# Optimization experiments

Measured on AMD Instinct MI355X. Metric: run time of the kernel, lower is better.

The kernel has to match this reference:

```python
import jax, jax.numpy as jnp
import numpy as np

N_E = 4096
E_DIM = 256
DECAY = 0.99
EPS = 1e-5


def setup_inputs() -> dict:
    key = jax.random.key(0)
    k1, k2 = jax.random.split(key)
    z = jax.random.normal(k1, (8, 256, 16, 16, 16), dtype=jnp.float32)
    embedding = jax.random.normal(k2, (N_E, E_DIM), dtype=jnp.float32)
    return {
        "z": z,
        "embedding": embedding,
        "cluster_size": jnp.zeros((N_E,), dtype=jnp.float32),
        "embedding_avg": embedding,  # buffer initialized as embedding.clone()
    }


def reference(z, embedding, cluster_size, embedding_avg):
    n_e, e_dim = embedding.shape
    # b c h w d -> b h w d c, then flatten tokens
    zt = jnp.einsum('bchwd->bhwdc', z)
    zf = zt.reshape(-1, e_dim)                      # [N, e_dim]
    # squared euclidean distances: ||z||^2 + ||e||^2 - 2 z.e
    d = (jnp.sum(zf * zf, axis=1, keepdims=True)
         + jnp.sum(embedding * embedding, axis=1)
         - 2.0 * jnp.einsum('bd,nd->bn', zf, embedding))  # [N, n_e]
    idx = jnp.argmin(d, axis=1)                     # [N]
    # EMA statistics (equivalent to one-hot.T reductions, done via scatter)
    n_total = jnp.zeros((n_e,), zf.dtype).at[idx].add(1.0)          # encodings.sum(0)
    dw = jax.ops.segment_sum(zf, idx, num_segments=n_e)             # encodings.T @ zf
    new_cluster = cluster_size * DECAY + (1.0 - DECAY) * n_total
    new_avg = embedding_avg * DECAY + (1.0 - DECAY) * dw
    n = new_cluster.sum()
    cs = (new_cluster + EPS) / (n + n_e * EPS) * n
    new_embed = new_avg / cs[:, None]
    # quantize (gather == one-hot @ embedding) with straight-through estimator
    zq = jnp.take(embedding, idx, axis=0).reshape(zt.shape)
    zq = zt + jax.lax.stop_gradient(zq - zt)
    zq = jnp.einsum('bhwdc->bchwd', zq)
    usage = (n_total > 0).sum().astype(jnp.float32) / n_e
    return zq, idx, new_cluster, new_avg, new_embed, usage
```

## Files before the change

### kernel.cpp

```cpp
#include <hip/hip_runtime.h>

#define N_E   4096
#define E_DIM 256
#define NTOK  32768
#define ZX    4096
#define DECAY 0.99f
#define EPSV  1e-5f
#define TAU   0.3f
#define NJB   32
#define NHALF 64
#define NSPL  4
#define IBIG  0x7fffffff

typedef _Float16 half8 __attribute__((ext_vector_type(8)));
typedef __attribute__((ext_vector_type(4))) float f32x4;

__device__ __forceinline__ unsigned short f2h(float x) {
    _Float16 h = (_Float16)x;
    unsigned short u;
    __builtin_memcpy(&u, &h, 2);
    return u;
}
__device__ __forceinline__ float h2f(unsigned short u) {
    _Float16 h;
    __builtin_memcpy(&h, &u, 2);
    return (float)h;
}
__device__ __forceinline__ unsigned umin2(unsigned a, unsigned b) { return a < b ? a : b; }
__device__ __forceinline__ unsigned umax2(unsigned a, unsigned b) { return a > b ? a : b; }
__device__ __forceinline__ void gload16(const void* g, void* l) {
    __builtin_amdgcn_global_load_lds(
        (const __attribute__((address_space(1))) char*)g,
        (__attribute__((address_space(3))) char*)l, 16, 0, 0);
}

__global__ void k_prep_z(const float* __restrict__ z, unsigned short* __restrict__ zh) {
    __shared__ float lt[64][65];
    const int bid = blockIdx.x;
    const int xt = bid & 63, ct = (bid >> 6) & 3, b = bid >> 8;
    const int tid = threadIdx.x;
    #pragma unroll
    for (int r = 0; r < 4; ++r) {
        int cy = r * 16 + (tid >> 4);
        int xx4 = tid & 15;
        float4 v = ((const float4*)z)[(size_t)(b * 256 + ct * 64 + cy) * 1024 + xt * 16 + xx4];
        lt[cy][xx4 * 4 + 0] = v.x; lt[cy][xx4 * 4 + 1] = v.y;
        lt[cy][xx4 * 4 + 2] = v.z; lt[cy][xx4 * 4 + 3] = v.w;
    }
    __syncthreads();
    #pragma unroll
    for (int it = 0; it < 2; ++it) {
        int tl = it * 32 + (tid >> 3);
        int c8 = tid & 7;
        unsigned short h[8];
        #pragma unroll
        for (int u = 0; u < 8; ++u) h[u] = f2h(lt[c8 * 8 + u][tl]);
        size_t t = (size_t)(b * 4096 + xt * 64 + tl);
        size_t o = t * 256 + ct * 64 + c8 * 8;
        *(ushort4*)&zh[o]     = make_ushort4(h[0], h[1], h[2], h[3]);
        *(ushort4*)&zh[o + 4] = make_ushort4(h[4], h[5], h[6], h[7]);
    }
}

__global__ void k_prep_e(const float* __restrict__ emb, unsigned short* __restrict__ Bp,
                         float* __restrict__ enorm32, double* __restrict__ enorm64,
                         int* __restrict__ cnt, int* __restrict__ flagCnt,
                         int* __restrict__ flagCnt2) {
    if (threadIdx.x < 4) cnt[blockIdx.x * 4 + threadIdx.x] = 0;
    if (blockIdx.x == 0 && threadIdx.x == 0) { *flagCnt = 0; *flagCnt2 = 0; }
    int j = blockIdx.x * 4 + (threadIdx.x >> 6);
    int lane = threadIdx.x & 63;
    float4 v = ((const float4*)emb)[(size_t)j * 64 + lane];
    float f[4] = {v.x, v.y, v.z, v.w};
    unsigned short h[4];
    #pragma unroll
    for (int u = 0; u < 4; ++u) h[u] = f2h(f[u]);
    *(ushort4*)&Bp[(size_t)j * E_DIM + lane * 4] = make_ushort4(h[0], h[1], h[2], h[3]);
    double s = 0.0;
    #pragma unroll
    for (int u = 0; u < 4; ++u) s += (double)f[u] * (double)f[u];
    #pragma unroll
    for (int off = 32; off; off >>= 1) s += __shfl_down(s, off, 64);
    if (lane == 0) { enorm32[j] = (float)s; enorm64[j] = s; }
}

__global__ __launch_bounds__(256) void k_dist(
        const unsigned short* __restrict__ zh,
        const unsigned short* __restrict__ Bp, const float* __restrict__ enorm32,
        unsigned* __restrict__ pk1, unsigned* __restrict__ pk2, unsigned* __restrict__ pk3) {
    __shared__ __align__(16) char smem[32768];
    const int tid = threadIdx.x;
    const int lane = tid & 63;
    const int w = tid >> 6;
    const int wr = w >> 1, wc = w & 1;
    const int t0 = blockIdx.x * 128;
    const int jb = blockIdx.y;
    const int j0 = jb * 128;
    const int sw16 = (((lane & 7) ^ (lane >> 3)) << 4);
    const int rowsub = lane >> 3;

    f32x4 acc[4][4];
    #pragma unroll
    for (int m = 0; m < 4; ++m)
        #pragma unroll
        for (int nn = 0; nn < 4; ++nn)
            acc[m][nn] = (f32x4){0.f, 0.f, 0.f, 0.f};

    auto stage = [&](int s) {
        const int kb = s * 128 + sw16;
        #pragma unroll
        for (int c = 0; c < 4; ++c) {
            int seg = w * 4 + c;
            int arow = t0 + seg * 8 + rowsub;
            int brow = j0 + seg * 8 + rowsub;
            gload16((const char*)zh + (size_t)arow * 512 + kb, &smem[seg * 1024]);
            gload16((const char*)Bp + (size_t)brow * 512 + kb, &smem[16384 + seg * 1024]);
        }
    };

    stage(0);
    for (int s = 0; s < 4; ++s) {
        __syncthreads();
        const int xr = ((lane & 7) << 4);
        #pragma unroll
        for (int kk = 0; kk < 2; ++kk) {
            const int colb = (kk * 64 + ((lane >> 4) << 4)) ^ xr;
            half8 a[4], b[4];
            #pragma unroll
            for (int m = 0; m < 4; ++m)
                a[m] = *(const half8*)&smem[((wr * 64 + m * 16 + (lane & 15)) << 7) + colb];
            #pragma unroll
            for (int nn = 0; nn < 4; ++nn)
                b[nn] = *(const half8*)&smem[16384 + ((wc * 64 + nn * 16 + (lane & 15)) << 7) + colb];
            #pragma unroll
            for (int m = 0; m < 4; ++m)
                #pragma unroll
                for (int nn = 0; nn < 4; ++nn)
                    acc[m][nn] = __builtin_amdgcn_mfma_f32_16x16x32_f16(b[nn], a[m], acc[m][nn], 0, 0, 0);
        }
        if (s < 3) {
            __syncthreads();
            stage(s + 1);
        }
    }

    const int g   = lane >> 4;
    const int gg4 = g * 4;
    const int h   = jb * 2 + wc;
    float enb[4][4];
    #pragma unroll
    for (int nn = 0; nn < 4; ++nn) {
        float4 e4 = *(const float4*)&enorm32[j0 + wc * 64 + nn * 16 + gg4];
        enb[nn][0] = e4.x + 4096.f; enb[nn][1] = e4.y + 4096.f;
        enb[nn][2] = e4.z + 4096.f; enb[nn][3] = e4.w + 4096.f;
    }
    unsigned s1 = 0, s2 = 0, s3 = 0;
    #pragma unroll
    for (int m = 0; m < 4; ++m) {
        unsigned k1 = 0xFFFFFFFFu, k2 = 0xFFFFFFFFu, k3 = 0xFFFFFFFFu;
        #pragma unroll
        for (int nn = 0; nn < 4; ++nn)
            #pragma unroll
            for (int r = 0; r < 4; ++r) {
                float sc = fmaf(-2.f, acc[m][nn][r], enb[nn][r]);
                unsigned key = (__float_as_uint(sc) & 0xFFFFFFC0u)
                             | (unsigned)(gg4 + nn * 16 + r);
                k3 = umin2(k3, umax2(k2, key));
                k2 = umin2(k2, umax2(k1, key));
                k1 = umin2(k1, key);
            }
        #pragma unroll
        for (int off = 16; off <= 32; off <<= 1) {
            unsigned b1 = (unsigned)__shfl_xor((int)k1, off, 64);
            unsigned b2 = (unsigned)__shfl_xor((int)k2, off, 64);
            unsigned b3 = (unsigned)__shfl_xor((int)k3, off, 64);
            unsigned p  = umax2(k1, b1);
            unsigned q  = umin2(k2, b2);
            unsigned r2 = umax2(k2, b2);
            unsigned ss = umin2(k3, b3);
            k1 = umin2(k1, b1);
            k2 = umin2(p, q);
            k3 = umin2(umax2(p, q), umin2(r2, ss));
        }
        s1 = (g == m) ? k1 : s1;
        s2 = (g == m) ? k2 : s2;
        s3 = (g == m) ? k3 : s3;
    }
    size_t o = (size_t)h * NTOK + t0 + wr * 64 + lane;
    pk1[o] = s1; pk2[o] = s2; pk3[o] = s3;
}

__global__ void k_merge(const unsigned* __restrict__ pk1, const unsigned* __restrict__ pk2,
                        const unsigned* __restrict__ pk3,
                        int* __restrict__ idx32, int* __restrict__ cnt,
                        float* __restrict__ out_idx,
                        int* __restrict__ xlist, int* __restrict__ xn,
                        int* __restrict__ flagList, int* __restrict__ flagCount,
                        int* __restrict__ flagList2, int* __restrict__ flagCount2) {
    int t = blockIdx.x * blockDim.x + threadIdx.x;
    if (t >= NTOK) return;
    unsigned g1 = 0xFFFFFFFFu, g2 = 0xFFFFFFFFu;
    int h1 = 0;
    for (int s = 0; s < NHALF; s++) {
        unsigned a = pk1[(size_t)s * NTOK + t];
        unsigned b = pk2[(size_t)s * NTOK + t];
        bool c = a < g1;
        g2 = c ? g1 : umin2(g2, a);
        h1 = c ? s : h1;
        g1 = c ? a : g1;
        g2 = umin2(g2, b);
    }
    int x1 = h1 * 64 + (int)(g1 & 63u);
    idx32[t] = x1;
    atomicAdd(&cnt[x1], 1);
    out_idx[t] = (float)x1;
    float v1 = __uint_as_float(g1 & 0xFFFFFFC0u);
    float v2 = __uint_as_float(g2 & 0xFFFFFFC0u);
    if (v2 - v1 >= TAU) return;
    unsigned thrk = __float_as_uint(v1 + TAU) | 63u;
    int nc = 0; bool full = false;
    for (int s = 0; s < NHALF; s++) {
        unsigned a = pk1[(size_t)s * NTOK + t];
        if (a > thrk) continue;
        if (pk3[(size_t)s * NTOK + t] <= thrk) { full = true; break; }
        if (nc == 8) { full = true; break; }
        xlist[t * 8 + nc++] = s * 64 + (int)(a & 63u);
        unsigned b = pk2[(size_t)s * NTOK + t];
        if (b <= thrk) {
            if (nc == 8) { full = true; break; }
            xlist[t * 8 + nc++] = s * 64 + (int)(b & 63u);
        }
    }
    if (full) {
        int q = atomicAdd(flagCount2, 1);
        flagList2[q] = t;
    } else {
        xn[t] = nc;
        int q = atomicAdd(flagCount, 1);
        flagList[q] = t;
    }
}

__global__ void k_tri(const float* __restrict__ z, const float* __restrict__ emb,
                      const double* __restrict__ enorm64,
                      const int* __restrict__ flagList, const int* __restrict__ flagCount,
                      const int* __restrict__ xlist, const int* __restrict__ xn,
                      int* __restrict__ idx32, int* __restrict__ cnt,
                      float* __restrict__ out_idx) {
    const int lane = threadIdx.x & 63;
    const int wid = blockIdx.x * (blockDim.x >> 6) + (threadIdx.x >> 6);
    const int nw = gridDim.x * (blockDim.x >> 6);
    const int nf = *flagCount;
    for (int f = wid; f < nf; f += nw) {
        int t = flagList[f];
        int b = t >> 12, x = t & 4095;
        double zz[4];
        #pragma unroll
        for (int u = 0; u < 4; ++u)
            zz[u] = (double)z[(size_t)(b * 256 + lane * 4 + u) * 4096 + x];
        int m = xn[t];
        double best = 1e300; int bi = IBIG;
        for (int c = 0; c < m; ++c) {
            int j = xlist[t * 8 + c];
            float4 e = ((const float4*)emb)[(size_t)j * 64 + lane];
            double d = zz[0] * (double)e.x + zz[1] * (double)e.y
                     + zz[2] * (double)e.z + zz[3] * (double)e.w;
            #pragma unroll
            for (int off = 32; off; off >>= 1) d += __shfl_down(d, off, 64);
            double s = enorm64[j] - 2.0 * d;
            if (s < best || (s == best && j < bi)) { best = s; bi = j; }
        }
        if (lane == 0) {
            int old = idx32[t];
            if (bi != old) {
                idx32[t] = bi;
                out_idx[t] = (float)bi;
                atomicSub(&cnt[old], 1);
                atomicAdd(&cnt[bi], 1);
            }
        }
    }
}

__global__ void k_recheck(const float* __restrict__ z, const float* __restrict__ emb,
                          const double* __restrict__ enorm64,
                          const int* __restrict__ flagList, const int* __restrict__ flagCount,
                          int* __restrict__ idx32, int* __restrict__ cnt,
                          float* __restrict__ out_idx) {
    __shared__ float zrow[E_DIM];
    __shared__ double rv[1024];
    __shared__ int ri[1024];
    const int tid = threadIdx.x;
    const int nf = *flagCount;
    for (int f = blockIdx.x; f < nf; f += gridDim.x) {
        const int t = flagList[f];
        const int b = t >> 12, x = t & 4095;
        __syncthreads();
        if (tid < E_DIM) zrow[tid] = z[(size_t)(b * 256 + tid) * 4096 + x];
        __syncthreads();
        double best = 1e300; int bi = IBIG;
        for (int s = 0; s < N_E / 1024; s++) {
            int j = s * 1024 + tid;
            const float4* er4 = (const float4*)(emb + (size_t)j * E_DIM);
            double a0 = 0.0, a1 = 0.0, a2 = 0.0, a3 = 0.0;
            for (int k4 = 0; k4 < 64; ++k4) {
                float4 e = er4[k4];
                a0 = fma((double)e.x, (double)zrow[k4 * 4 + 0], a0);
                a1 = fma((double)e.y, (double)zrow[k4 * 4 + 1], a1);
                a2 = fma((double)e.z, (double)zrow[k4 * 4 + 2], a2);
                a3 = fma((double)e.w, (double)zrow[k4 * 4 + 3], a3);
            }
            double d = enorm64[j] - 2.0 * ((a0 + a1) + (a2 + a3));
            if (d < best || (d == best && j < bi)) { best = d; bi = j; }
        }
        rv[tid] = best; ri[tid] = bi;
        __syncthreads();
        for (int off = 512; off; off >>= 1) {
            if (tid < off) {
                if (rv[tid + off] < rv[tid] ||
                    (rv[tid + off] == rv[tid] && ri[tid + off] < ri[tid])) {
                    rv[tid] = rv[tid + off]; ri[tid] = ri[tid + off];
                }
            }
            __syncthreads();
        }
        if (tid == 0) {
            int old = idx32[t];
            int nw = ri[0];
            if (nw != old) {
                idx32[t] = nw;
                out_idx[t] = (float)nw;
                atomicSub(&cnt[old], 1);
                atomicAdd(&cnt[nw], 1);
            }
        }
        __syncthreads();
    }
}

__global__ void k_scan(const int* __restrict__ cnt, int* __restrict__ offs,
                       const float* __restrict__ cluster_size,
                       float* __restrict__ nval, float* __restrict__ out_usage) {
    __shared__ int sc[1024];
    __shared__ float sn[1024];
    __shared__ float su[1024];
    int tid = threadIdx.x;
    int c0 = cnt[tid * 4], c1 = cnt[tid * 4 + 1], c2 = cnt[tid * 4 + 2], c3 = cnt[tid * 4 + 3];
    int ls = c0 + c1 + c2 + c3;
    float ns = 0.f, us = 0.f;
    {
        int cc[4] = {c0, c1, c2, c3};
        #pragma unroll
        for (int u = 0; u < 4; ++u) {
            ns += cluster_size[tid * 4 + u] * DECAY + (1.f - DECAY) * (float)cc[u];
            us += (cc[u] > 0) ? 1.f : 0.f;
        }
    }
    sc[tid] = ls; sn[tid] = ns; su[tid] = us;
    __syncthreads();
    for (int off = 1; off < 1024; off <<= 1) {
        int v = (tid >= off) ? sc[tid - off] : 0;
        __syncthreads();
        sc[tid] += v;
        __syncthreads();
    }
    int base = sc[tid] - ls;
    offs[tid * 4] = base;
    offs[tid * 4 + 1] = base + c0;
    offs[tid * 4 + 2] = base + c0 + c1;
    offs[tid * 4 + 3] = base + c0 + c1 + c2;
    for (int off = 512; off; off >>= 1) {
        if (tid < off) { sn[tid] += sn[tid + off]; su[tid] += su[tid + off]; }
        __syncthreads();
    }
    if (tid == 0) { *nval = sn[0]; *out_usage = su[0] / (float)N_E; }
}

__global__ void k_place(const int* __restrict__ idx32, int* __restrict__ offs,
                        int* __restrict__ tokList) {
    int t = blockIdx.x * blockDim.x + threadIdx.x;
    if (t >= NTOK) return;
    int j = idx32[t];
    int p = atomicAdd(&offs[j], 1);
    tokList[p] = t;
}

__global__ __launch_bounds__(512) void k_dw(const unsigned short* __restrict__ zh,
                       const int* __restrict__ cnt, const int* __restrict__ offs,
                       const int* __restrict__ tokList, float* __restrict__ dwp) {
    __shared__ float red[8][256];
    const int j = blockIdx.x;
    const int split = blockIdx.y;
    const int g = threadIdx.x >> 6;
    const int lane = threadIdx.x & 63;
    const int n = cnt[j];
    const int s0 = offs[j] - n;
    const int stride = NSPL * 8;
    float4 acc = make_float4(0.f, 0.f, 0.f, 0.f);
    int i = split * 8 + g;
    if (i < n) {
        int t_cur = tokList[s0 + i];
        i += stride;
        for (; i < n; i += stride) {
            int t_nxt = tokList[s0 + i];
            ushort4 h = *(const ushort4*)&zh[(size_t)t_cur * 256 + lane * 4];
            acc.x += h2f(h.x); acc.y += h2f(h.y);
            acc.z += h2f(h.z); acc.w += h2f(h.w);
            t_cur = t_nxt;
        }
        ushort4 h = *(const ushort4*)&zh[(size_t)t_cur * 256 + lane * 4];
        acc.x += h2f(h.x); acc.y += h2f(h.y);
        acc.z += h2f(h.z); acc.w += h2f(h.w);
    }
    red[g][lane * 4 + 0] = acc.x; red[g][lane * 4 + 1] = acc.y;
    red[g][lane * 4 + 2] = acc.z; red[g][lane * 4 + 3] = acc.w;
    __syncthreads();
    if (g == 0) {
        float4 o;
        int c = lane * 4;
        o.x = red[0][c+0] + red[1][c+0] + red[2][c+0] + red[3][c+0]
            + red[4][c+0] + red[5][c+0] + red[6][c+0] + red[7][c+0];
        o.y = red[0][c+1] + red[1][c+1] + red[2][c+1] + red[3][c+1]
            + red[4][c+1] + red[5][c+1] + red[6][c+1] + red[7][c+1];
        o.z = red[0][c+2] + red[1][c+2] + red[2][c+2] + red[3][c+2]
            + red[4][c+2] + red[5][c+2] + red[6][c+2] + red[7][c+2];
        o.w = red[0][c+3] + red[1][c+3] + red[2][c+3] + red[3][c+3]
            + red[4][c+3] + red[5][c+3] + red[6][c+3] + red[7][c+3];
        ((float4*)dwp)[((size_t)split * N_E + j) * 64 + lane] = o;
    }
}

__global__ void k_final(const float* __restrict__ dwp, const int* __restrict__ cnt,
                        const float* __restrict__ cluster_size,
                        const float* __restrict__ emb_avg, const float* __restrict__ nval,
                        float* __restrict__ out_cluster, float* __restrict__ out_avg,
                        float* __restrict__ out_embed) {
    int j = blockIdx.x * 4 + (threadIdx.x >> 6);
    int lane = threadIdx.x & 63;
    float4 dw = make_float4(0.f, 0.f, 0.f, 0.f);
    #pragma unroll
    for (int s = 0; s < NSPL; ++s) {
        float4 v = ((const float4*)dwp)[((size_t)s * N_E + j) * 64 + lane];
        dw.x += v.x; dw.y += v.y; dw.z += v.z; dw.w += v.w;
    }
    float nc = cluster_size[j] * DECAY + (1.f - DECAY) * (float)cnt[j];
    float nv = *nval;
    float cs = (nc + EPSV) / (nv + (float)N_E * EPSV) * nv;
    float4 ea = ((const float4*)emb_avg)[(size_t)j * 64 + lane];
    float4 na, ne;
    na.x = ea.x * DECAY + (1.f - DECAY) * dw.x;
    na.y = ea.y * DECAY + (1.f - DECAY) * dw.y;
    na.z = ea.z * DECAY + (1.f - DECAY) * dw.z;
    na.w = ea.w * DECAY + (1.f - DECAY) * dw.w;
    ne.x = na.x / cs; ne.y = na.y / cs; ne.z = na.z / cs; ne.w = na.w / cs;
    ((float4*)out_avg)[(size_t)j * 64 + lane] = na;
    ((float4*)out_embed)[(size_t)j * 64 + lane] = ne;
    if (lane == 0) out_cluster[j] = nc;
}

__global__ void k_zq(const float* __restrict__ emb, const int* __restrict__ idx32,
                     float* __restrict__ out_zq) {
    int t0 = blockIdx.x * 16;
    int b = t0 >> 12, x0 = t0 & 4095;
    int c4 = threadIdx.x >> 2;
    int xq = threadIdx.x & 3;
    int jj[4];
    #pragma unroll
    for (int i = 0; i < 4; ++i) jj[i] = idx32[t0 + xq * 4 + i];
    float4 e[4];
    #pragma unroll
    for (int i = 0; i < 4; ++i)
        e[i] = ((const float4*)emb)[(size_t)jj[i] * 64 + c4];
    float* ob = out_zq + (size_t)b * (E_DIM * ZX) + x0 + xq * 4;
    {
        float4 v = make_float4(e[0].x, e[1].x, e[2].x, e[3].x);
        *(float4*)&ob[(size_t)(c4 * 4 + 0) * ZX] = v;
    }
    {
        float4 v = make_float4(e[0].y, e[1].y, e[2].y, e[3].y);
        *(float4*)&ob[(size_t)(c4 * 4 + 1) * ZX] = v;
    }
    {
        float4 v = make_float4(e[0].z, e[1].z, e[2].z, e[3].z);
        *(float4*)&ob[(size_t)(c4 * 4 + 2) * ZX] = v;
    }
    {
        float4 v = make_float4(e[0].w, e[1].w, e[2].w, e[3].w);
        *(float4*)&ob[(size_t)(c4 * 4 + 3) * ZX] = v;
    }
}

extern "C" void kernel_launch(void* const* d_in, const int* in_sizes, int n_in,
                              void* d_out, int out_size, void* d_ws, size_t ws_size,
                              hipStream_t stream) {
    const float* z            = (const float*)d_in[0];
    const float* emb          = (const float*)d_in[1];
    const float* cluster_size = (const float*)d_in[2];
    const float* emb_avg      = (const float*)d_in[3];
    float* out = (float*)d_out;

    char* ws = (char*)d_ws;
    unsigned short* zh   = (unsigned short*)(ws + 0);
    float* enorm32       = (float*)(ws + 16777216);
    double* enorm64      = (double*)(ws + 16793600);
    int* idx32           = (int*)(ws + 16826368);
    int* flagList        = (int*)(ws + 16957440);
    int* flagList2       = (int*)(ws + 17088512);
    int* xlist           = (int*)(ws + 17219584);
    int* xn              = (int*)(ws + 18268160);
    int* cnt             = (int*)(ws + 18399232);
    int* offs            = (int*)(ws + 18415616);
    int* flagCnt         = (int*)(ws + 18432000);
    int* flagCnt2        = (int*)(ws + 18432064);
    float* nval          = (float*)(ws + 18432128);

    unsigned* pk1        = (unsigned*)(out + 0);
    unsigned* pk2        = (unsigned*)(out + 2097152);
    unsigned* pk3        = (unsigned*)(out + 4194304);
    float* dwp           = out + 0;
    unsigned short* Bp   = (unsigned short*)(out + 7340032);
    int*   tokList       = (int*)(out + 7864320);

    float* out_zq      = out + 0;
    float* out_idx     = out + 8388608;
    float* out_cluster = out + 8421376;
    float* out_avg     = out + 8425472;
    float* out_embed   = out + 9474048;
    float* out_usage   = out + 10522624;

    hipLaunchKernelGGL(k_prep_z, dim3(2048), dim3(256), 0, stream, z, zh);
    hipLaunchKernelGGL(k_prep_e, dim3(1024), dim3(256), 0, stream, emb, Bp, enorm32, enorm64,
                       cnt, flagCnt, flagCnt2);
    hipLaunchKernelGGL(k_dist,   dim3(256, NJB), dim3(256), 0, stream,
                       zh, Bp, enorm32, pk1, pk2, pk3);
    hipLaunchKernelGGL(k_merge,  dim3(128), dim3(256), 0, stream,
                       pk1, pk2, pk3, idx32, cnt, out_idx,
                       xlist, xn, flagList, flagCnt, flagList2, flagCnt2);
    hipLaunchKernelGGL(k_tri,    dim3(512), dim3(256), 0, stream,
                       z, emb, enorm64, flagList, flagCnt, xlist, xn, idx32, cnt, out_idx);
    hipLaunchKernelGGL(k_recheck, dim3(128), dim3(1024), 0, stream,
                       z, emb, enorm64, flagList2, flagCnt2, idx32, cnt, out_idx);
    hipLaunchKernelGGL(k_scan,   dim3(1), dim3(1024), 0, stream, cnt, offs,
                       cluster_size, nval, out_usage);
    hipLaunchKernelGGL(k_place,  dim3(128), dim3(256), 0, stream, idx32, offs, tokList);
    hipLaunchKernelGGL(k_dw,     dim3(4096, NSPL), dim3(512), 0, stream,
                       zh, cnt, offs, tokList, dwp);
    hipLaunchKernelGGL(k_final,  dim3(1024), dim3(256), 0, stream,
                       dwp, cnt, cluster_size, emb_avg, nval,
                       out_cluster, out_avg, out_embed);
    hipLaunchKernelGGL(k_zq,     dim3(2048), dim3(256), 0, stream, emb, idx32, out_zq);
}
```

Measured before the change: 201.7 us.

## Merge prep, refinement, and final/zq kernels to cut launch count

Result: no change. 199.8 us (-1.0%).

```diff
diff --git a/kernel.cpp b/kernel.cpp
--- a/kernel.cpp
+++ b/kernel.cpp
@@ -34,54 +34,56 @@
         (__attribute__((address_space(3))) char*)l, 16, 0, 0);
 }
 
-__global__ void k_prep_z(const float* __restrict__ z, unsigned short* __restrict__ zh) {
+__global__ void k_prep(const float* __restrict__ z, unsigned short* __restrict__ zh,
+                       const float* __restrict__ emb, unsigned short* __restrict__ Bp,
+                       float* __restrict__ enorm32, double* __restrict__ enorm64,
+                       int* __restrict__ cnt, int* __restrict__ flagCnt,
+                       int* __restrict__ flagCnt2) {
     __shared__ float lt[64][65];
-    const int bid = blockIdx.x;
-    const int xt = bid & 63, ct = (bid >> 6) & 3, b = bid >> 8;
     const int tid = threadIdx.x;
-    #pragma unroll
-    for (int r = 0; r < 4; ++r) {
-        int cy = r * 16 + (tid >> 4);
-        int xx4 = tid & 15;
-        float4 v = ((const float4*)z)[(size_t)(b * 256 + ct * 64 + cy) * 1024 + xt * 16 + xx4];
-        lt[cy][xx4 * 4 + 0] = v.x; lt[cy][xx4 * 4 + 1] = v.y;
-        lt[cy][xx4 * 4 + 2] = v.z; lt[cy][xx4 * 4 + 3] = v.w;
-    }
-    __syncthreads();
-    #pragma unroll
-    for (int it = 0; it < 2; ++it) {
-        int tl = it * 32 + (tid >> 3);
-        int c8 = tid & 7;
-        unsigned short h[8];
-        #pragma unroll
-        for (int u = 0; u < 8; ++u) h[u] = f2h(lt[c8 * 8 + u][tl]);
-        size_t t = (size_t)(b * 4096 + xt * 64 + tl);
-        size_t o = t * 256 + ct * 64 + c8 * 8;
-        *(ushort4*)&zh[o]     = make_ushort4(h[0], h[1], h[2], h[3]);
-        *(ushort4*)&zh[o + 4] = make_ushort4(h[4], h[5], h[6], h[7]);
-    }
-}
-
-__global__ void k_prep_e(const float* __restrict__ emb, unsigned short* __restrict__ Bp,
-                         float* __restrict__ enorm32, double* __restrict__ enorm64,
-                         int* __restrict__ cnt, int* __restrict__ flagCnt,
-                         int* __restrict__ flagCnt2) {
-    if (threadIdx.x < 4) cnt[blockIdx.x * 4 + threadIdx.x] = 0;
-    if (blockIdx.x == 0 && threadIdx.x == 0) { *flagCnt = 0; *flagCnt2 = 0; }
-    int j = blockIdx.x * 4 + (threadIdx.x >> 6);
-    int lane = threadIdx.x & 63;
-    float4 v = ((const float4*)emb)[(size_t)j * 64 + lane];
-    float f[4] = {v.x, v.y, v.z, v.w};
-    unsigned short h[4];
-    #pragma unroll
-    for (int u = 0; u < 4; ++u) h[u] = f2h(f[u]);
-    *(ushort4*)&Bp[(size_t)j * E_DIM + lane * 4] = make_ushort4(h[0], h[1], h[2], h[3]);
-    double s = 0.0;
-    #pragma unroll
-    for (int u = 0; u < 4; ++u) s += (double)f[u] * (double)f[u];
-    #pragma unroll
-    for (int off = 32; off; off >>= 1) s += __shfl_down(s, off, 64);
-    if (lane == 0) { enorm32[j] = (float)s; enorm64[j] = s; }
+    if (blockIdx.x < 2048) {
+        const int bid = blockIdx.x;
+        const int xt = bid & 63, ct = (bid >> 6) & 3, b = bid >> 8;
+        #pragma unroll
+        for (int r = 0; r < 4; ++r) {
+            int cy = r * 16 + (tid >> 4);
+            int xx4 = tid & 15;
+            float4 v = ((const float4*)z)[(size_t)(b * 256 + ct * 64 + cy) * 1024 + xt * 16 + xx4];
+            lt[cy][xx4 * 4 + 0] = v.x; lt[cy][xx4 * 4 + 1] = v.y;
+            lt[cy][xx4 * 4 + 2] = v.z; lt[cy][xx4 * 4 + 3] = v.w;
+        }
+        __syncthreads();
+        #pragma unroll
+        for (int it = 0; it < 2; ++it) {
+            int tl = it * 32 + (tid >> 3);
+            int c8 = tid & 7;
+            unsigned short h[8];
+            #pragma unroll
+            for (int u = 0; u < 8; ++u) h[u] = f2h(lt[c8 * 8 + u][tl]);
+            size_t t = (size_t)(b * 4096 + xt * 64 + tl);
+            size_t o = t * 256 + ct * 64 + c8 * 8;
+            *(ushort4*)&zh[o]     = make_ushort4(h[0], h[1], h[2], h[3]);
+            *(ushort4*)&zh[o + 4] = make_ushort4(h[4], h[5], h[6], h[7]);
+        }
+    } else {
+        const int eb = blockIdx.x - 2048;
+        if (tid < 4) cnt[eb * 4 + tid] = 0;
+        if (eb == 0 && tid == 0) { *flagCnt = 0; *flagCnt2 = 0; }
+        int j = eb * 4 + (tid >> 6);
+        int lane = tid & 63;
+        float4 v = ((const float4*)emb)[(size_t)j * 64 + lane];
+        float f[4] = {v.x, v.y, v.z, v.w};
+        unsigned short h[4];
+        #pragma unroll
+        for (int u = 0; u < 4; ++u) h[u] = f2h(f[u]);
+        *(ushort4*)&Bp[(size_t)j * E_DIM + lane * 4] = make_ushort4(h[0], h[1], h[2], h[3]);
+        double s = 0.0;
+        #pragma unroll
+        for (int u = 0; u < 4; ++u) s += (double)f[u] * (double)f[u];
+        #pragma unroll
+        for (int off = 32; off; off >>= 1) s += __shfl_down(s, off, 64);
+        if (lane == 0) { enorm32[j] = (float)s; enorm64[j] = s; }
+    }
 }
 
 __global__ __launch_bounds__(256) void k_dist(
@@ -201,6 +203,7 @@
     if (t >= NTOK) return;
     unsigned g1 = 0xFFFFFFFFu, g2 = 0xFFFFFFFFu;
     int h1 = 0;
+    #pragma unroll 4
     for (int s = 0; s < NHALF; s++) {
         unsigned a = pk1[(size_t)s * NTOK + t];
         unsigned b = pk2[(size_t)s * NTOK + t];
@@ -241,100 +244,97 @@
     }
 }
 
-__global__ void k_tri(const float* __restrict__ z, const float* __restrict__ emb,
-                      const double* __restrict__ enorm64,
-                      const int* __restrict__ flagList, const int* __restrict__ flagCount,
-                      const int* __restrict__ xlist, const int* __restrict__ xn,
-                      int* __restrict__ idx32, int* __restrict__ cnt,
-                      float* __restrict__ out_idx) {
-    const int lane = threadIdx.x & 63;
-    const int wid = blockIdx.x * (blockDim.x >> 6) + (threadIdx.x >> 6);
-    const int nw = gridDim.x * (blockDim.x >> 6);
-    const int nf = *flagCount;
-    for (int f = wid; f < nf; f += nw) {
-        int t = flagList[f];
-        int b = t >> 12, x = t & 4095;
-        double zz[4];
-        #pragma unroll
-        for (int u = 0; u < 4; ++u)
-            zz[u] = (double)z[(size_t)(b * 256 + lane * 4 + u) * 4096 + x];
-        int m = xn[t];
-        double best = 1e300; int bi = IBIG;
-        for (int c = 0; c < m; ++c) {
-            int j = xlist[t * 8 + c];
-            float4 e = ((const float4*)emb)[(size_t)j * 64 + lane];
-            double d = zz[0] * (double)e.x + zz[1] * (double)e.y
-                     + zz[2] * (double)e.z + zz[3] * (double)e.w;
+__global__ __launch_bounds__(512) void k_triR(
+        const float* __restrict__ z, const float* __restrict__ emb,
+        const double* __restrict__ enorm64,
+        const int* __restrict__ flagList, const int* __restrict__ flagCount,
+        const int* __restrict__ xlist, const int* __restrict__ xn,
+        const int* __restrict__ flagList2, const int* __restrict__ flagCount2,
+        int* __restrict__ idx32, int* __restrict__ cnt, float* __restrict__ out_idx) {
+    __shared__ float zrow[E_DIM];
+    __shared__ double rv[512];
+    __shared__ int ri[512];
+    const int tid = threadIdx.x;
+    if (blockIdx.x < 384) {
+        const int lane = tid & 63;
+        const int wid = blockIdx.x * 8 + (tid >> 6);
+        const int nw = 384 * 8;
+        const int nf = *flagCount;
+        for (int f = wid; f < nf; f += nw) {
+            int t = flagList[f];
+            int b = t >> 12, x = t & 4095;
+            double zz[4];
             #pragma unroll
-            for (int off = 32; off; off >>= 1) d += __shfl_down(d, off, 64);
-            double s = enorm64[j] - 2.0 * d;
-            if (s < best || (s == best && j < bi)) { best = s; bi = j; }
-        }
-        if (lane == 0) {
-            int old = idx32[t];
-            if (bi != old) {
-                idx32[t] = bi;
-                out_idx[t] = (float)bi;
-                atomicSub(&cnt[old], 1);
-                atomicAdd(&cnt[bi], 1);
+            for (int u = 0; u < 4; ++u)
+                zz[u] = (double)z[(size_t)(b * 256 + lane * 4 + u) * 4096 + x];
+            int m = xn[t];
+            double best = 1e300; int bi = IBIG;
+            for (int c = 0; c < m; ++c) {
+                int j = xlist[t * 8 + c];
+                float4 e = ((const float4*)emb)[(size_t)j * 64 + lane];
+                double d = zz[0] * (double)e.x + zz[1] * (double)e.y
+                         + zz[2] * (double)e.z + zz[3] * (double)e.w;
+                #pragma unroll
+                for (int off = 32; off; off >>= 1) d += __shfl_down(d, off, 64);
+                double s = enorm64[j] - 2.0 * d;
+                if (s < best || (s == best && j < bi)) { best = s; bi = j; }
             }
-        }
-    }
-}
-
-__global__ void k_recheck(const float* __restrict__ z, const float* __restrict__ emb,
-                          const double* __restrict__ enorm64,
-                          const int* __restrict__ flagList, const int* __restrict__ flagCount,
-                          int* __restrict__ idx32, int* __restrict__ cnt,
-                          float* __restrict__ out_idx) {
-    __shared__ float zrow[E_DIM];
-    __shared__ double rv[1024];
-    __shared__ int ri[1024];
-    const int tid = threadIdx.x;
-    const int nf = *flagCount;
-    for (int f = blockIdx.x; f < nf; f += gridDim.x) {
-        const int t = flagList[f];
-        const int b = t >> 12, x = t & 4095;
-        __syncthreads();
-        if (tid < E_DIM) zrow[tid] = z[(size_t)(b * 256 + tid) * 4096 + x];
-        __syncthreads();
-        double best = 1e300; int bi = IBIG;
-        for (int s = 0; s < N_E / 1024; s++) {
-            int j = s * 1024 + tid;
-            const float4* er4 = (const float4*)(emb + (size_t)j * E_DIM);
-            double a0 = 0.0, a1 = 0.0, a2 = 0.0, a3 = 0.0;
-            for (int k4 = 0; k4 < 64; ++k4) {
-                float4 e = er4[k4];
-                a0 = fma((double)e.x, (double)zrow[k4 * 4 + 0], a0);
-                a1 = fma((double)e.y, (double)zrow[k4 * 4 + 1], a1);
-                a2 = fma((double)e.z, (double)zrow[k4 * 4 + 2], a2);
-                a3 = fma((double)e.w, (double)zrow[k4 * 4 + 3], a3);
+            if (lane == 0) {
+                int old = idx32[t];
+                if (bi != old) {
+                    idx32[t] = bi;
+                    out_idx[t] = (float)bi;
+                    atomicSub(&cnt[old], 1);
+                    atomicAdd(&cnt[bi], 1);
+                }
             }
-            double d = enorm64[j] - 2.0 * ((a0 + a1) + (a2 + a3));
-            if (d < best || (d == best && j < bi)) { best = d; bi = j; }
-        }
-        rv[tid] = best; ri[tid] = bi;
-        __syncthreads();
-        for (int off = 512; off; off >>= 1) {
-            if (tid < off) {
-                if (rv[tid + off] < rv[tid] ||
-                    (rv[tid + off] == rv[tid] && ri[tid + off] < ri[tid])) {
-                    rv[tid] = rv[tid + off]; ri[tid] = ri[tid + off];
+        }
+    } else {
+        const int nf = *flagCount2;
+        for (int f = blockIdx.x - 384; f < nf; f += 128) {
+            const int t = flagList2[f];
+            const int b = t >> 12, x = t & 4095;
+            __syncthreads();
+            if (tid < E_DIM) zrow[tid] = z[(size_t)(b * 256 + tid) * 4096 + x];
+            __syncthreads();
+            double best = 1e300; int bi = IBIG;
+            for (int s = 0; s < N_E / 512; s++) {
+                int j = s * 512 + tid;
+                const float4* er4 = (const float4*)(emb + (size_t)j * E_DIM);
+                double a0 = 0.0, a1 = 0.0, a2 = 0.0, a3 = 0.0;
+                for (int k4 = 0; k4 < 64; ++k4) {
+                    float4 e = er4[k4];
+                    a0 = fma((double)e.x, (double)zrow[k4 * 4 + 0], a0);
+                    a1 = fma((double)e.y, (double)zrow[k4 * 4 + 1], a1);
+                    a2 = fma((double)e.z, (double)zrow[k4 * 4 + 2], a2);
+                    a3 = fma((double)e.w, (double)zrow[k4 * 4 + 3], a3);
+                }
+                double d = enorm64[j] - 2.0 * ((a0 + a1) + (a2 + a3));
+                if (d < best || (d == best && j < bi)) { best = d; bi = j; }
+            }
+            rv[tid] = best; ri[tid] = bi;
+            __syncthreads();
+            for (int off = 256; off; off >>= 1) {
+                if (tid < off) {
+                    if (rv[tid + off] < rv[tid] ||
+                        (rv[tid + off] == rv[tid] && ri[tid + off] < ri[tid])) {
+                        rv[tid] = rv[tid + off]; ri[tid] = ri[tid + off];
+                    }
+                }
+                __syncthreads();
+            }
+            if (tid == 0) {
+                int old = idx32[t];
+                int nw2 = ri[0];
+                if (nw2 != old) {
+                    idx32[t] = nw2;
+                    out_idx[t] = (float)nw2;
+                    atomicSub(&cnt[old], 1);
+                    atomicAdd(&cnt[nw2], 1);
                 }
             }
             __syncthreads();
         }
-        if (tid == 0) {
-            int old = idx32[t];
-            int nw = ri[0];
-            if (nw != old) {
-                idx32[t] = nw;
-                out_idx[t] = (float)nw;
-                atomicSub(&cnt[old], 1);
-                atomicAdd(&cnt[nw], 1);
-            }
-        }
-        __syncthreads();
     }
 }
 
@@ -430,63 +430,49 @@
     }
 }
 
-__global__ void k_final(const float* __restrict__ dwp, const int* __restrict__ cnt,
-                        const float* __restrict__ cluster_size,
-                        const float* __restrict__ emb_avg, const float* __restrict__ nval,
-                        float* __restrict__ out_cluster, float* __restrict__ out_avg,
-                        float* __restrict__ out_embed) {
-    int j = blockIdx.x * 4 + (threadIdx.x >> 6);
-    int lane = threadIdx.x & 63;
-    float4 dw = make_float4(0.f, 0.f, 0.f, 0.f);
-    #pragma unroll
-    for (int s = 0; s < NSPL; ++s) {
-        float4 v = ((const float4*)dwp)[((size_t)s * N_E + j) * 64 + lane];
-        dw.x += v.x; dw.y += v.y; dw.z += v.z; dw.w += v.w;
-    }
-    float nc = cluster_size[j] * DECAY + (1.f - DECAY) * (float)cnt[j];
-    float nv = *nval;
-    float cs = (nc + EPSV) / (nv + (float)N_E * EPSV) * nv;
-    float4 ea = ((const float4*)emb_avg)[(size_t)j * 64 + lane];
-    float4 na, ne;
-    na.x = ea.x * DECAY + (1.f - DECAY) * dw.x;
-    na.y = ea.y * DECAY + (1.f - DECAY) * dw.y;
-    na.z = ea.z * DECAY + (1.f - DECAY) * dw.z;
-    na.w = ea.w * DECAY + (1.f - DECAY) * dw.w;
-    ne.x = na.x / cs; ne.y = na.y / cs; ne.z = na.z / cs; ne.w = na.w / cs;
-    ((float4*)out_avg)[(size_t)j * 64 + lane] = na;
-    ((float4*)out_embed)[(size_t)j * 64 + lane] = ne;
-    if (lane == 0) out_cluster[j] = nc;
-}
-
-__global__ void k_zq(const float* __restrict__ emb, const int* __restrict__ idx32,
-                     float* __restrict__ out_zq) {
-    int t0 = blockIdx.x * 16;
-    int b = t0 >> 12, x0 = t0 & 4095;
-    int c4 = threadIdx.x >> 2;
-    int xq = threadIdx.x & 3;
-    int jj[4];
-    #pragma unroll
-    for (int i = 0; i < 4; ++i) jj[i] = idx32[t0 + xq * 4 + i];
-    float4 e[4];
-    #pragma unroll
-    for (int i = 0; i < 4; ++i)
-        e[i] = ((const float4*)emb)[(size_t)jj[i] * 64 + c4];
-    float* ob = out_zq + (size_t)b * (E_DIM * ZX) + x0 + xq * 4;
-    {
-        float4 v = make_float4(e[0].x, e[1].x, e[2].x, e[3].x);
-        *(float4*)&ob[(size_t)(c4 * 4 + 0) * ZX] = v;
-    }
-    {
-        float4 v = make_float4(e[0].y, e[1].y, e[2].y, e[3].y);
-        *(float4*)&ob[(size_t)(c4 * 4 + 1) * ZX] = v;
-    }
-    {
-        float4 v = make_float4(e[0].z, e[1].z, e[2].z, e[3].z);
-        *(float4*)&ob[(size_t)(c4 * 4 + 2) * ZX] = v;
-    }
-    {
-        float4 v = make_float4(e[0].w, e[1].w, e[2].w, e[3].w);
-        *(float4*)&ob[(size_t)(c4 * 4 + 3) * ZX] = v;
+__global__ void k_finalzq(const float* __restrict__ dwp, const int* __restrict__ cnt,
+                          const float* __restrict__ cluster_size,
+                          const float* __restrict__ emb_avg, const float* __restrict__ nval,
+                          float* __restrict__ out_cluster, float* __restrict__ out_avg,
+                          float* __restrict__ out_embed,
+                          const float* __restrict__ emb, const int* __restrict__ idx32,
+                          float* __restrict__ out_zq) {
+    if (blockIdx.x < 1024) {
+        int j = blockIdx.x * 4 + (threadIdx.x >> 6);
+        int lane = threadIdx.x & 63;
+        float4 dw = make_float4(0.f, 0.f, 0.f, 0.f);
+        #pragma unroll
+        for (int s = 0; s < NSPL; ++s) {
+            float4 v = ((const float4*)dwp)[((size_t)s * N_E + j) * 64 + lane];
+            dw.x += v.x; dw.y += v.y; dw.z += v.z; dw.w += v.w;
+        }
+        float nc = cluster_size[j] * DECAY + (1.f - DECAY) * (float)cnt[j];
+        float nv = *nval;
+        float cs = (nc + EPSV) / (nv + (float)N_E * EPSV) * nv;
+        float4 ea = ((const float4*)emb_avg)[(size_t)j * 64 + lane];
+        float4 na, ne;
+        na.x = ea.x * DECAY + (1.f - DECAY) * dw.x;
+        na.y = ea.y * DECAY + (1.f - DECAY) * dw.y;
+        na.z = ea.z * DECAY + (1.f - DECAY) * dw.z;
+        na.w = ea.w * DECAY + (1.f - DECAY) * dw.w;
+        ne.x = na.x / cs; ne.y = na.y / cs; ne.z = na.z / cs; ne.w = na.w / cs;
+        ((float4*)out_avg)[(size_t)j * 64 + lane] = na;
+        ((float4*)out_embed)[(size_t)j * 64 + lane] = ne;
+        if (lane == 0) out_cluster[j] = nc;
+    } else {
+        int t = (blockIdx.x - 1024) * 256 + threadIdx.x;
+        int j = idx32[t];
+        int b = t >> 12, x = t & 4095;
+        const float4* er = (const float4*)(emb + (size_t)j * E_DIM);
+        float* ob = out_zq + (size_t)b * (E_DIM * ZX) + x;
+        #pragma unroll 8
+        for (int c4 = 0; c4 < E_DIM / 4; c4++) {
+            float4 v = er[c4];
+            ob[(size_t)(c4 * 4 + 0) * ZX] = v.x;
+            ob[(size_t)(c4 * 4 + 1) * ZX] = v.y;
+            ob[(size_t)(c4 * 4 + 2) * ZX] = v.z;
+            ob[(size_t)(c4 * 4 + 3) * ZX] = v.w;
+        }
     }
 }
 
@@ -513,11 +499,11 @@
     int* flagCnt         = (int*)(ws + 18432000);
     int* flagCnt2        = (int*)(ws + 18432064);
     float* nval          = (float*)(ws + 18432128);
+    float* dwp           = (float*)(ws + 18874368);
 
     unsigned* pk1        = (unsigned*)(out + 0);
     unsigned* pk2        = (unsigned*)(out + 2097152);
     unsigned* pk3        = (unsigned*)(out + 4194304);
-    float* dwp           = out + 0;
     unsigned short* Bp   = (unsigned short*)(out + 7340032);
     int*   tokList       = (int*)(out + 7864320);
 
@@ -528,25 +514,22 @@
     float* out_embed   = out + 9474048;
     float* out_usage   = out + 10522624;
 
-    hipLaunchKernelGGL(k_prep_z, dim3(2048), dim3(256), 0, stream, z, zh);
-    hipLaunchKernelGGL(k_prep_e, dim3(1024), dim3(256), 0, stream, emb, Bp, enorm32, enorm64,
-                       cnt, flagCnt, flagCnt2);
+    hipLaunchKernelGGL(k_prep,   dim3(3072), dim3(256), 0, stream,
+                       z, zh, emb, Bp, enorm32, enorm64, cnt, flagCnt, flagCnt2);
     hipLaunchKernelGGL(k_dist,   dim3(256, NJB), dim3(256), 0, stream,
                        zh, Bp, enorm32, pk1, pk2, pk3);
     hipLaunchKernelGGL(k_merge,  dim3(128), dim3(256), 0, stream,
                        pk1, pk2, pk3, idx32, cnt, out_idx,
                        xlist, xn, flagList, flagCnt, flagList2, flagCnt2);
-    hipLaunchKernelGGL(k_tri,    dim3(512), dim3(256), 0, stream,
-                       z, emb, enorm64, flagList, flagCnt, xlist, xn, idx32, cnt, out_idx);
-    hipLaunchKernelGGL(k_recheck, dim3(128), dim3(1024), 0, stream,
-                       z, emb, enorm64, flagList2, flagCnt2, idx32, cnt, out_idx);
+    hipLaunchKernelGGL(k_triR,   dim3(512), dim3(512), 0, stream,
+                       z, emb, enorm64, flagList, flagCnt, xlist, xn,
+                       flagList2, flagCnt2, idx32, cnt, out_idx);
     hipLaunchKernelGGL(k_scan,   dim3(1), dim3(1024), 0, stream, cnt, offs,
                        cluster_size, nval, out_usage);
     hipLaunchKernelGGL(k_place,  dim3(128), dim3(256), 0, stream, idx32, offs, tokList);
     hipLaunchKernelGGL(k_dw,     dim3(4096, NSPL), dim3(512), 0, stream,
                        zh, cnt, offs, tokList, dwp);
-    hipLaunchKernelGGL(k_final,  dim3(1024), dim3(256), 0, stream,
+    hipLaunchKernelGGL(k_finalzq, dim3(1152), dim3(256), 0, stream,
                        dwp, cnt, cluster_size, emb_avg, nval,
-                       out_cluster, out_avg, out_embed);
-    hipLaunchKernelGGL(k_zq,     dim3(2048), dim3(256), 0, stream, emb, idx32, out_zq);
-}
+                       out_cluster, out_avg, out_embed, emb, idx32, out_zq);
+}
```
